# Performance work log

Measured on AMD Instinct MI355X. Metric: run time of the kernel, lower is better.

## Reference

```python
import jax, jax.numpy as jnp
import numpy as np

EPS_MIN = 1e-8
N_ITER = 50  # solver_iter


def solve_qp_simplex(M, n_iter=N_ITER):
    """Frank-Wolfe min over the simplex of alpha^T M alpha. M: (B,K,K) -> alpha: (B,K)."""
    B, K, _ = M.shape
    alpha0 = jnp.full((B, K), 1.0 / K, dtype=M.dtype)

    def step(alpha, it):
        grad = 2.0 * jnp.einsum('bij,bj->bi', M, alpha)           # (B,K)
        idx = jnp.argmin(grad, axis=1)                             # (B,)
        s = jax.nn.one_hot(idx, K, dtype=alpha.dtype)              # vertex of simplex
        gamma = 2.0 / (it + 2.0)
        return (1.0 - gamma) * alpha + gamma * s, None

    alpha, _ = jax.lax.scan(step, alpha0, jnp.arange(n_iter, dtype=M.dtype))
    return alpha


def _raw_loss(scores, targets, C):
    B, K = scores.shape
    # epsilon = offdiag_mean of C per batch, scaled by 1.0, clamped
    offdiag_mean = (C.sum(axis=(1, 2)) - jnp.trace(C, axis1=1, axis2=2)) / (K * K - K)
    eps = jnp.maximum(offdiag_mean, EPS_MIN)                       # (B,)

    f = 0.5 * scores
    exponent = -(f[:, :, None] + f[:, None, :] + C) / eps[:, None, None]  # (B,K,K)
    shift = exponent.max(axis=(1, 2), keepdims=True)
    logM = exponent - shift
    M = jnp.exp(logM)

    # solver is an implicit layer: non-differentiable by construction
    alpha = jax.lax.stop_gradient(solve_qp_simplex(M, N_ITER))     # (B,K)

    pos = alpha > 0
    loga = jnp.where(pos, jnp.log(jnp.where(pos, alpha, 1.0)), -jnp.inf)
    term = loga[:, :, None] + loga[:, None, :] + logM              # (B,K,K)
    logval = jax.scipy.special.logsumexp(term.reshape(B, K * K), axis=1)
    conjugate = -eps * (logval + shift.reshape(B))

    f_y = jnp.take_along_axis(scores, targets[:, None], axis=1)[:, 0]
    return conjugate - f_y


def setup_inputs() -> dict:
    key = jax.random.key(0)
    k1, k2, k3 = jax.random.split(key, 3)
    B, K = 512, 256
    scores = jax.random.normal(k1, (B, K), dtype=jnp.float32)
    targets = jax.random.randint(k2, (B,), 0, K)
    C = jax.random.uniform(k3, (B, K, K), dtype=jnp.float32)
    return {"scores": scores, "targets": targets, "C": C}


def reference(scores, targets, C):
    return _raw_loss(scores, targets, C).mean()
```

## Files before the change

### kernel.cpp

```cpp
#include <hip/hip_runtime.h>
#include <hip/hip_fp16.h>
#include <math.h>

#define KDIM 256
#define NITER 50
#define REG_H 8192
#define STR 266


__global__ __launch_bounds__(256, 8) void k1_partials(
    const float* __restrict__ scores, const float* __restrict__ C,
    float* __restrict__ psum_o, float* __restrict__ ptrace_o, float* __restrict__ pmin_o)
{
    const int blk = blockIdx.x;
    const int b = blk >> 2, chunk = blk & 3;
    const int tid = threadIdx.x, lane = tid & 63, wave = tid >> 6;
    const float4* C4 = (const float4*)(C + (size_t)b * KDIM * KDIM);

    __shared__ float sf[KDIM];
    __shared__ float redS[256], redT[256], redM[256];
    sf[tid] = 0.5f * scores[b*KDIM + tid];
    __syncthreads();

    const int j0 = lane * 4;
    const float fj0 = sf[j0], fj1 = sf[j0+1], fj2 = sf[j0+2], fj3 = sf[j0+3];

    const int row0 = chunk * 64;
    float psum = 0.f, ptrace = 0.f, pmin = INFINITY;
    #pragma unroll
    for (int rr = 0; rr < 16; ++rr) {
        const int row = row0 + wave + rr*4;
        float4 c4 = C4[row*(KDIM/4) + lane];
        const float frow = sf[row];
        psum += (c4.x + c4.y) + (c4.z + c4.w);
        pmin = fminf(pmin, fminf(fminf(frow+fj0+c4.x, frow+fj1+c4.y),
                                 fminf(frow+fj2+c4.z, frow+fj3+c4.w)));
        if ((row >> 2) == lane) {
            int r2 = row & 3;
            ptrace += (r2==0)?c4.x:(r2==1)?c4.y:(r2==2)?c4.z:c4.w;
        }
    }
    redS[tid] = psum; redT[tid] = ptrace; redM[tid] = pmin;
    __syncthreads();
    for (int s = 128; s > 0; s >>= 1) {
        if (tid < s) {
            redS[tid] += redS[tid+s];
            redT[tid] += redT[tid+s];
            redM[tid]  = fminf(redM[tid], redM[tid+s]);
        }
        __syncthreads();
    }
    if (tid == 0) { psum_o[blk] = redS[0]; ptrace_o[blk] = redT[0]; pmin_o[blk] = redM[0]; }
}

__global__ __launch_bounds__(256, 7) void k2_trowsum(
    const float* __restrict__ scores, const float* __restrict__ C,
    const float* __restrict__ psum_i, const float* __restrict__ ptrace_i, const float* __restrict__ pmin_i,
    __half* __restrict__ CT, float* __restrict__ rs)
{
    const int blk = blockIdx.x;
    const int b = blk >> 2, chunk = blk & 3;
    const int tid = threadIdx.x, lane = tid & 63, wave = tid >> 6;
    const float4* C4 = (const float4*)(C + (size_t)b * KDIM * KDIM);
    __half* CTb = CT + (size_t)((b*4 + chunk) * 2) * REG_H;

    __shared__ float sf[KDIM];
    __shared__ __half T[32 * STR];
    __shared__ float part[12];
    __shared__ float bc2[2];

    sf[tid] = 0.5f * scores[b*KDIM + tid];
    if (tid < 12) {
        part[tid] = (tid < 4) ? psum_i[b*4+tid]
                  : (tid < 8) ? ptrace_i[b*4+tid-4]
                              : pmin_i[b*4+tid-8];
    }
    __syncthreads();
    if (tid == 0) {
        float s = part[0]+part[1]+part[2]+part[3];
        float t = part[4]+part[5]+part[6]+part[7];
        float mn = fminf(fminf(part[8],part[9]), fminf(part[10],part[11]));
        bc2[0] = mn;
        bc2[1] = fmaxf((s - t) / (float)(KDIM*KDIM - KDIM), 1e-8f);
    }
    __syncthreads();
    const float minv = bc2[0];
    const float inv_eps = 1.0f / bc2[1];

    const int j0 = lane * 4;
    const float fj0 = sf[j0], fj1 = sf[j0+1], fj2 = sf[j0+2], fj3 = sf[j0+3];

    #pragma unroll
    for (int p = 0; p < 2; ++p) {
        #pragma unroll
        for (int it = 0; it < 8; ++it) {
            const int sl  = it*4 + wave;
            const int row = chunk*64 + p*32 + sl;
            float4 c4 = C4[row*(KDIM/4) + lane];
            const float base = minv - sf[row];
            float s4 = __expf((base - fj0 - c4.x) * inv_eps)
                     + __expf((base - fj1 - c4.y) * inv_eps)
                     + __expf((base - fj2 - c4.z) * inv_eps)
                     + __expf((base - fj3 - c4.w) * inv_eps);
            #pragma unroll
            for (int off = 32; off > 0; off >>= 1) s4 += __shfl_xor(s4, off);
            if (lane == 0) rs[b*KDIM + row] = s4;
            __half2 h01, h23;
            h01.x = __float2half_rn(c4.x); h01.y = __float2half_rn(c4.y);
            h23.x = __float2half_rn(c4.z); h23.y = __float2half_rn(c4.w);
            *(__half2*)&T[sl*STR + j0    ] = h01;
            *(__half2*)&T[sl*STR + j0 + 2] = h23;
        }
        __syncthreads();
        {
            __half* dst = CTb + (size_t)p * REG_H;
            const int jr  = tid >> 2;
            const int sl0 = (tid & 3) * 8;
            #pragma unroll
            for (int r = 0; r < 4; ++r) {
                const int j = r*64 + jr;
                uint w[4];
                #pragma unroll
                for (int dw = 0; dw < 4; ++dw) {
                    const uint u0 = (uint)__half_as_ushort(T[(sl0 + dw*2    )*STR + j]);
                    const uint u1 = (uint)__half_as_ushort(T[(sl0 + dw*2 + 1)*STR + j]);
                    w[dw] = u0 | (u1 << 16);
                }
                uint4 v; v.x = w[0]; v.y = w[1]; v.z = w[2]; v.w = w[3];
                *(uint4*)(dst + (size_t)j*32 + sl0) = v;
            }
        }
        __syncthreads();
    }
}

__global__ __launch_bounds__(256) void k3_fw(
    const float* __restrict__ scores, const int* __restrict__ targets,
    const __half* __restrict__ CT,
    const float* __restrict__ psum_i, const float* __restrict__ ptrace_i, const float* __restrict__ pmin_i,
    const float* __restrict__ rs, float* __restrict__ lossB)
{
    const int b = blockIdx.x;
    const int tid = threadIdx.x, lane = tid & 63, wave = tid >> 6;
    const __half* CTb = CT + (size_t)b * 8 * REG_H;

    __shared__ float sf[KDIM];
    __shared__ float part[12];
    __shared__ float bc2[2];
    __shared__ float rsL[KDIM];
    __shared__ float aAll[KDIM];
    __shared__ int   wcnt[4];
    __shared__ int   sIdx[64];
    __shared__ float sLog[64];
    __shared__ float wm[4], wsm[4];

    sf[tid] = 0.5f * scores[b*KDIM + tid];
    if (tid < 12) {
        part[tid] = (tid < 4) ? psum_i[b*4+tid]
                  : (tid < 8) ? ptrace_i[b*4+tid-4]
                              : pmin_i[b*4+tid-8];
    }
    rsL[tid] = rs[b*KDIM + tid];
    __syncthreads();
    if (tid == 0) {
        float s = part[0]+part[1]+part[2]+part[3];
        float t = part[4]+part[5]+part[6]+part[7];
        float mn = fminf(fminf(part[8],part[9]), fminf(part[10],part[11]));
        bc2[0] = mn;
        bc2[1] = fmaxf((s - t) / (float)(KDIM*KDIM - KDIM), 1e-8f);
    }
    __syncthreads();
    const float minv = bc2[0];
    const float eps = bc2[1];
    const float inv_eps = 1.0f / eps;

    if (wave == 0) {
        const float f0 = sf[lane], f1 = sf[lane+64], f2 = sf[lane+128], f3 = sf[lane+192];
        const __half* g0p = CTb + (size_t)(0*2 + (lane>>5))*REG_H + (lane&31);
        const __half* g1p = CTb + (size_t)(1*2 + (lane>>5))*REG_H + (lane&31);
        const __half* g2p = CTb + (size_t)(2*2 + (lane>>5))*REG_H + (lane&31);
        const __half* g3p = CTb + (size_t)(3*2 + (lane>>5))*REG_H + (lane&31);

        float v = rsL[lane]; int vi = lane;
        float t;
        t = rsL[lane+64];  if (t < v) { v = t; vi = lane+64; }
        t = rsL[lane+128]; if (t < v) { v = t; vi = lane+128; }
        t = rsL[lane+192]; if (t < v) { v = t; vi = lane+192; }
        #pragma unroll
        for (int off = 32; off > 0; off >>= 1) {
            float ov = __shfl_xor(v, off);
            int  ovi = __shfl_xor(vi, off);
            if (ov < v || (ov == v && ovi < vi)) { v = ov; vi = ovi; }
        }
        const int idx0 = vi;

        float fidx = sf[idx0];
        float g0 = 2.0f * __expf((minv - (f0 + fidx + __half2float(g0p[(size_t)idx0*32]))) * inv_eps);
        float g1 = 2.0f * __expf((minv - (f1 + fidx + __half2float(g1p[(size_t)idx0*32]))) * inv_eps);
        float g2 = 2.0f * __expf((minv - (f2 + fidx + __half2float(g2p[(size_t)idx0*32]))) * inv_eps);
        float g3 = 2.0f * __expf((minv - (f3 + fidx + __half2float(g3p[(size_t)idx0*32]))) * inv_eps);
        float a0 = (lane     == idx0) ? 1.0f : 0.0f;
        float a1 = (lane+64  == idx0) ? 1.0f : 0.0f;
        float a2 = (lane+128 == idx0) ? 1.0f : 0.0f;
        float a3 = (lane+192 == idx0) ? 1.0f : 0.0f;

        for (int it = 1; it < NITER; ++it) {
            float v2 = g0; int vi2 = lane;
            if (g1 < v2) { v2 = g1; vi2 = lane+64; }
            if (g2 < v2) { v2 = g2; vi2 = lane+128; }
            if (g3 < v2) { v2 = g3; vi2 = lane+192; }
            #pragma unroll
            for (int off = 32; off > 0; off >>= 1) {
                float ov = __shfl_xor(v2, off);
                int  ovi = __shfl_xor(vi2, off);
                if (ov < v2 || (ov == v2 && ovi < vi2)) { v2 = ov; vi2 = ovi; }
            }
            const int idx = vi2;
            const float gamma = 2.0f / ((float)it + 2.0f);
            const float omg = 1.0f - gamma;
            const int which = idx >> 6;
            float fsel = (which==0) ? f0 : (which==1) ? f1 : (which==2) ? f2 : f3;
            const float fidx2 = __shfl(fsel, idx & 63);
            const size_t co = (size_t)idx * 32;
            const float cc0 = __half2float(g0p[co]);
            const float cc1 = __half2float(g1p[co]);
            const float cc2 = __half2float(g2p[co]);
            const float cc3 = __half2float(g3p[co]);
            g0 = omg*g0 + 2.0f*gamma*__expf((minv - (f0 + fidx2 + cc0)) * inv_eps);
            g1 = omg*g1 + 2.0f*gamma*__expf((minv - (f1 + fidx2 + cc1)) * inv_eps);
            g2 = omg*g2 + 2.0f*gamma*__expf((minv - (f2 + fidx2 + cc2)) * inv_eps);
            g3 = omg*g3 + 2.0f*gamma*__expf((minv - (f3 + fidx2 + cc3)) * inv_eps);
            a0 = omg*a0 + ((lane     == idx) ? gamma : 0.0f);
            a1 = omg*a1 + ((lane+64  == idx) ? gamma : 0.0f);
            a2 = omg*a2 + ((lane+128 == idx) ? gamma : 0.0f);
            a3 = omg*a3 + ((lane+192 == idx) ? gamma : 0.0f);
        }
        aAll[lane]     = a0;
        aAll[lane+64]  = a1;
        aAll[lane+128] = a2;
        aAll[lane+192] = a3;
    }
    __syncthreads();

    const float a = aAll[tid];

    unsigned long long mask = __ballot(a > 0.f);
    if (lane == 0) wcnt[wave] = __popcll(mask);
    __syncthreads();
    int off0 = 0;
    for (int w = 0; w < wave; ++w) off0 += wcnt[w];
    const int count = wcnt[0] + wcnt[1] + wcnt[2] + wcnt[3];
    if (a > 0.f) {
        int pos = off0 + __popcll(mask & ((1ull << lane) - 1ull));
        sIdx[pos] = tid;
        sLog[pos] = logf(a);
    }
    __syncthreads();

    float m = -INFINITY, ss = 0.f;
    const int total = count * count;
    for (int p = tid; p < total; p += KDIM) {
        int ii = p / count;
        int jj = p - ii * count;
        int i = sIdx[ii], j = sIdx[jj];
        float cij = __half2float(CTb[(size_t)((i>>6)*2 + ((i>>5)&1))*REG_H + (size_t)j*32 + (i&31)]);
        float lm = (minv - (sf[i] + sf[j] + cij)) * inv_eps;
        float tt = sLog[ii] + sLog[jj] + lm;
        if (tt > m) { ss = ss * __expf(m - tt) + 1.0f; m = tt; }
        else        { ss += __expf(tt - m); }
    }
    #pragma unroll
    for (int off = 32; off > 0; off >>= 1) {
        float om = __shfl_xor(m, off);
        float os = __shfl_xor(ss, off);
        if (os > 0.f) {
            if (ss <= 0.f)   { m = om; ss = os; }
            else if (om > m) { ss = ss*__expf(m-om) + os; m = om; }
            else             { ss += os*__expf(om-m); }
        }
    }
    if (lane == 0) { wm[wave] = m; wsm[wave] = ss; }
    __syncthreads();
    if (tid == 0) {
        float M = wm[0], S = wsm[0];
        #pragma unroll
        for (int w = 1; w < 4; ++w) {
            float om = wm[w], os = wsm[w];
            if (os > 0.f) {
                if (S <= 0.f)    { M = om; S = os; }
                else if (om > M) { S = S*__expf(M-om) + os; M = om; }
                else             { S += os*__expf(om-M); }
            }
        }
        float logval = M + logf(S);
        float shift = -minv * inv_eps;
        float conjugate = -eps * (logval + shift);
        float fy = scores[b*KDIM + targets[b]];
        lossB[b] = conjugate - fy;
    }
}

__global__ __launch_bounds__(512) void cacis_reduce(const float* __restrict__ lossB,
                                                    float* __restrict__ out, int B)
{
    __shared__ float red[512];
    int t = threadIdx.x;
    red[t] = (t < B) ? lossB[t] : 0.f;
    __syncthreads();
    for (int s = 256; s > 0; s >>= 1) { if (t < s) red[t] += red[t+s]; __syncthreads(); }
    if (t == 0) out[0] = red[0] / (float)B;
}

extern "C" void kernel_launch(void* const* d_in, const int* in_sizes, int n_in,
                              void* d_out, int out_size, void* d_ws, size_t ws_size,
                              hipStream_t stream) {
    const float* scores  = (const float*)d_in[0];
    const int*   targets = (const int*)d_in[1];
    const float* C       = (const float*)d_in[2];
    float* out = (float*)d_out;
    const int B = in_sizes[1];

    __half* CT  = (__half*)d_ws;
    float* wsf  = (float*)((char*)d_ws + (size_t)67108864);
    float* psum   = wsf;
    float* ptrace = wsf + 2048;
    float* pmin   = wsf + 4096;
    float* rs     = wsf + 6144;
    float* lossB  = wsf + 6144 + 131072;

    k1_partials<<<B*4, 256, 0, stream>>>(scores, C, psum, ptrace, pmin);
    k2_trowsum <<<B*4, 256, 0, stream>>>(scores, C, psum, ptrace, pmin, CT, rs);
    k3_fw      <<<B,   256, 0, stream>>>(scores, targets, CT, psum, ptrace, pmin, rs, lossB);
    cacis_reduce<<<1, 512, 0, stream>>>(lossB, out, B);
}
```

Measured before the change: 124.0 us.

## Drop fp16 transposed copy of C; read C directly in Frank-Wolfe loop

The second kernel no longer writes a transposed half-precision copy of C to workspace. It now computes per-column-chunk partial row sums of M from a shared-memory tile and writes them as four partials that the solver kernel adds up. The solver kernel reads the original fp32 C rows with strided gathers, both in the 50 iterations and in the final logsumexp. This removes a 64MB workspace write and its later reads, but each Frank-Wolfe step now does scattered 4-byte loads across rows of C instead of reading a contiguous transposed layout.

```diff
diff --git a/kernel.cpp b/kernel.cpp
--- a/kernel.cpp
+++ b/kernel.cpp
@@ -4,8 +4,6 @@
 
 #define KDIM 256
 #define NITER 50
-#define REG_H 8192
-#define STR 266
 
 
 __global__ __launch_bounds__(256, 8) void k1_partials(
@@ -53,21 +51,21 @@
     if (tid == 0) { psum_o[blk] = redS[0]; ptrace_o[blk] = redT[0]; pmin_o[blk] = redM[0]; }
 }
 
-__global__ __launch_bounds__(256, 7) void k2_trowsum(
+#define TSTR 66
+__global__ __launch_bounds__(256, 4) void k2_rowsums(
     const float* __restrict__ scores, const float* __restrict__ C,
     const float* __restrict__ psum_i, const float* __restrict__ ptrace_i, const float* __restrict__ pmin_i,
-    __half* __restrict__ CT, float* __restrict__ rs)
+    float* __restrict__ prs)
 {
     const int blk = blockIdx.x;
-    const int b = blk >> 2, chunk = blk & 3;
-    const int tid = threadIdx.x, lane = tid & 63, wave = tid >> 6;
+    const int b = blk >> 2, jc = blk & 3;
+    const int tid = threadIdx.x;
     const float4* C4 = (const float4*)(C + (size_t)b * KDIM * KDIM);
-    __half* CTb = CT + (size_t)((b*4 + chunk) * 2) * REG_H;
 
     __shared__ float sf[KDIM];
-    __shared__ __half T[32 * STR];
     __shared__ float part[12];
     __shared__ float bc2[2];
+    __shared__ __half tile[KDIM * TSTR];
 
     sf[tid] = 0.5f * scores[b*KDIM + tid];
     if (tid < 12) {
@@ -87,62 +85,43 @@
     const float minv = bc2[0];
     const float inv_eps = 1.0f / bc2[1];
 
-    const int j0 = lane * 4;
-    const float fj0 = sf[j0], fj1 = sf[j0+1], fj2 = sf[j0+2], fj3 = sf[j0+3];
-
+    const int rsub = tid >> 4;
+    const int cq   = tid & 15;
     #pragma unroll
-    for (int p = 0; p < 2; ++p) {
-        #pragma unroll
-        for (int it = 0; it < 8; ++it) {
-            const int sl  = it*4 + wave;
-            const int row = chunk*64 + p*32 + sl;
-            float4 c4 = C4[row*(KDIM/4) + lane];
-            const float base = minv - sf[row];
-            float s4 = __expf((base - fj0 - c4.x) * inv_eps)
-                     + __expf((base - fj1 - c4.y) * inv_eps)
-                     + __expf((base - fj2 - c4.z) * inv_eps)
-                     + __expf((base - fj3 - c4.w) * inv_eps);
-            #pragma unroll
-            for (int off = 32; off > 0; off >>= 1) s4 += __shfl_xor(s4, off);
-            if (lane == 0) rs[b*KDIM + row] = s4;
-            __half2 h01, h23;
-            h01.x = __float2half_rn(c4.x); h01.y = __float2half_rn(c4.y);
-            h23.x = __float2half_rn(c4.z); h23.y = __float2half_rn(c4.w);
-            *(__half2*)&T[sl*STR + j0    ] = h01;
-            *(__half2*)&T[sl*STR + j0 + 2] = h23;
-        }
-        __syncthreads();
-        {
-            __half* dst = CTb + (size_t)p * REG_H;
-            const int jr  = tid >> 2;
-            const int sl0 = (tid & 3) * 8;
-            #pragma unroll
-            for (int r = 0; r < 4; ++r) {
-                const int j = r*64 + jr;
-                uint w[4];
-                #pragma unroll
-                for (int dw = 0; dw < 4; ++dw) {
-                    const uint u0 = (uint)__half_as_ushort(T[(sl0 + dw*2    )*STR + j]);
-                    const uint u1 = (uint)__half_as_ushort(T[(sl0 + dw*2 + 1)*STR + j]);
-                    w[dw] = u0 | (u1 << 16);
-                }
-                uint4 v; v.x = w[0]; v.y = w[1]; v.z = w[2]; v.w = w[3];
-                *(uint4*)(dst + (size_t)j*32 + sl0) = v;
-            }
-        }
-        __syncthreads();
-    }
+    for (int k = 0; k < 16; ++k) {
+        const int row = k*16 + rsub;
+        float4 c4 = C4[row*(KDIM/4) + jc*16 + cq];
+        __half2 h01, h23;
+        h01.x = __float2half_rn(c4.x); h01.y = __float2half_rn(c4.y);
+        h23.x = __float2half_rn(c4.z); h23.y = __float2half_rn(c4.w);
+        *(__half2*)&tile[row*TSTR + cq*4    ] = h01;
+        *(__half2*)&tile[row*TSTR + cq*4 + 2] = h23;
+    }
+    __syncthreads();
+
+    const float base = minv - sf[tid];
+    const __half* rowp = &tile[tid*TSTR];
+    float acc = 0.f;
+    #pragma unroll
+    for (int c = 0; c < 32; ++c) {
+        __half2 h = *(const __half2*)&rowp[c*2];
+        const float fja = sf[jc*64 + c*2];
+        const float fjb = sf[jc*64 + c*2 + 1];
+        acc += __expf((base - fja - __half2float(h.x)) * inv_eps)
+             + __expf((base - fjb - __half2float(h.y)) * inv_eps);
+    }
+    prs[(size_t)blk*KDIM + tid] = acc;
 }
 
 __global__ __launch_bounds__(256) void k3_fw(
     const float* __restrict__ scores, const int* __restrict__ targets,
-    const __half* __restrict__ CT,
+    const float* __restrict__ C,
     const float* __restrict__ psum_i, const float* __restrict__ ptrace_i, const float* __restrict__ pmin_i,
-    const float* __restrict__ rs, float* __restrict__ lossB)
+    const float* __restrict__ prs, float* __restrict__ lossB)
 {
     const int b = blockIdx.x;
     const int tid = threadIdx.x, lane = tid & 63, wave = tid >> 6;
-    const __half* CTb = CT + (size_t)b * 8 * REG_H;
+    const float* Cb = C + (size_t)b * KDIM * KDIM;
 
     __shared__ float sf[KDIM];
     __shared__ float part[12];
@@ -160,7 +139,8 @@
                   : (tid < 8) ? ptrace_i[b*4+tid-4]
                               : pmin_i[b*4+tid-8];
     }
-    rsL[tid] = rs[b*KDIM + tid];
+    rsL[tid] = prs[(size_t)(b*4+0)*KDIM+tid] + prs[(size_t)(b*4+1)*KDIM+tid]
+             + prs[(size_t)(b*4+2)*KDIM+tid] + prs[(size_t)(b*4+3)*KDIM+tid];
     __syncthreads();
     if (tid == 0) {
         float s = part[0]+part[1]+part[2]+part[3];
@@ -176,10 +156,10 @@
 
     if (wave == 0) {
         const float f0 = sf[lane], f1 = sf[lane+64], f2 = sf[lane+128], f3 = sf[lane+192];
-        const __half* g0p = CTb + (size_t)(0*2 + (lane>>5))*REG_H + (lane&31);
-        const __half* g1p = CTb + (size_t)(1*2 + (lane>>5))*REG_H + (lane&31);
-        const __half* g2p = CTb + (size_t)(2*2 + (lane>>5))*REG_H + (lane&31);
-        const __half* g3p = CTb + (size_t)(3*2 + (lane>>5))*REG_H + (lane&31);
+        const float* r0 = Cb + (size_t)lane*KDIM;
+        const float* r1 = r0 + 64*KDIM;
+        const float* r2 = r0 + 128*KDIM;
+        const float* r3 = r0 + 192*KDIM;
 
         float v = rsL[lane]; int vi = lane;
         float t;
@@ -195,10 +175,10 @@
         const int idx0 = vi;
 
         float fidx = sf[idx0];
-        float g0 = 2.0f * __expf((minv - (f0 + fidx + __half2float(g0p[(size_t)idx0*32]))) * inv_eps);
-        float g1 = 2.0f * __expf((minv - (f1 + fidx + __half2float(g1p[(size_t)idx0*32]))) * inv_eps);
-        float g2 = 2.0f * __expf((minv - (f2 + fidx + __half2float(g2p[(size_t)idx0*32]))) * inv_eps);
-        float g3 = 2.0f * __expf((minv - (f3 + fidx + __half2float(g3p[(size_t)idx0*32]))) * inv_eps);
+        float g0 = 2.0f * __expf((minv - (f0 + fidx + r0[idx0])) * inv_eps);
+        float g1 = 2.0f * __expf((minv - (f1 + fidx + r1[idx0])) * inv_eps);
+        float g2 = 2.0f * __expf((minv - (f2 + fidx + r2[idx0])) * inv_eps);
+        float g3 = 2.0f * __expf((minv - (f3 + fidx + r3[idx0])) * inv_eps);
         float a0 = (lane     == idx0) ? 1.0f : 0.0f;
         float a1 = (lane+64  == idx0) ? 1.0f : 0.0f;
         float a2 = (lane+128 == idx0) ? 1.0f : 0.0f;
@@ -221,11 +201,7 @@
             const int which = idx >> 6;
             float fsel = (which==0) ? f0 : (which==1) ? f1 : (which==2) ? f2 : f3;
             const float fidx2 = __shfl(fsel, idx & 63);
-            const size_t co = (size_t)idx * 32;
-            const float cc0 = __half2float(g0p[co]);
-            const float cc1 = __half2float(g1p[co]);
-            const float cc2 = __half2float(g2p[co]);
-            const float cc3 = __half2float(g3p[co]);
+            const float cc0 = r0[idx], cc1 = r1[idx], cc2 = r2[idx], cc3 = r3[idx];
             g0 = omg*g0 + 2.0f*gamma*__expf((minv - (f0 + fidx2 + cc0)) * inv_eps);
             g1 = omg*g1 + 2.0f*gamma*__expf((minv - (f1 + fidx2 + cc1)) * inv_eps);
             g2 = omg*g2 + 2.0f*gamma*__expf((minv - (f2 + fidx2 + cc2)) * inv_eps);
@@ -263,7 +239,7 @@
         int ii = p / count;
         int jj = p - ii * count;
         int i = sIdx[ii], j = sIdx[jj];
-        float cij = __half2float(CTb[(size_t)((i>>6)*2 + ((i>>5)&1))*REG_H + (size_t)j*32 + (i&31)]);
+        float cij = Cb[i*KDIM + j];
         float lm = (minv - (sf[i] + sf[j] + cij)) * inv_eps;
         float tt = sLog[ii] + sLog[jj] + lm;
         if (tt > m) { ss = ss * __expf(m - tt) + 1.0f; m = tt; }
@@ -320,16 +296,15 @@
     float* out = (float*)d_out;
     const int B = in_sizes[1];
 
-    __half* CT  = (__half*)d_ws;
-    float* wsf  = (float*)((char*)d_ws + (size_t)67108864);
-    float* psum   = wsf;
-    float* ptrace = wsf + 2048;
-    float* pmin   = wsf + 4096;
-    float* rs     = wsf + 6144;
-    float* lossB  = wsf + 6144 + 131072;
+    float* ws     = (float*)d_ws;
+    float* psum   = ws;
+    float* ptrace = ws + 2048;
+    float* pmin   = ws + 4096;
+    float* prs    = ws + 6144;
+    float* lossB  = ws + 6144 + 524288;
 
     k1_partials<<<B*4, 256, 0, stream>>>(scores, C, psum, ptrace, pmin);
-    k2_trowsum <<<B*4, 256, 0, stream>>>(scores, C, psum, ptrace, pmin, CT, rs);
-    k3_fw      <<<B,   256, 0, stream>>>(scores, targets, CT, psum, ptrace, pmin, rs, lossB);
+    k2_rowsums <<<B*4, 256, 0, stream>>>(scores, C, psum, ptrace, pmin, prs);
+    k3_fw      <<<B,   256, 0, stream>>>(scores, targets, C, psum, ptrace, pmin, prs, lossB);
     cacis_reduce<<<1, 512, 0, stream>>>(lossB, out, B);
 }
```

Result: slower. 131.6 us (+6.1%).
